# Kernel optimization log

Hardware: AMD Instinct MI355X
Metric: run time of the kernel (lower is better)

## Reference

```python
import jax, jax.numpy as jnp
import numpy as np

N_NODES = 100000
N_EDGES = 1600000
EMBED_DIM = 64


def setup_inputs() -> dict:
    key = jax.random.key(0)
    k1, k2, k3, k4 = jax.random.split(key, 4)
    ego_embeddings = jax.random.normal(k1, (N_NODES, EMBED_DIM), dtype=jnp.float32)
    adj_values = jax.random.uniform(k2, (N_EDGES,), dtype=jnp.float32)
    adj_rows = jax.random.randint(k3, (N_EDGES,), 0, N_NODES, dtype=jnp.int32)
    adj_cols = jax.random.randint(k4, (N_EDGES,), 0, N_NODES, dtype=jnp.int32)
    return {
        "ego_embeddings": ego_embeddings,
        "adj_values": adj_values,
        "adj_rows": adj_rows,
        "adj_cols": adj_cols,
    }


def reference(ego_embeddings, adj_values, adj_rows, adj_cols):
    # out[r, :] = sum_{e : rows[e]==r} values[e] * ego_embeddings[cols[e], :]
    # == tf.sparse.sparse_dense_matmul(adj, ego_embeddings)
    messages = adj_values[:, None] * ego_embeddings[adj_cols]  # [E, D]
    out = jax.ops.segment_sum(messages, adj_rows, num_segments=N_NODES)  # [N, D]
    return out
```

## Files before the change

kernel.cpp:

```cpp
#include <hip/hip_runtime.h>

#define N_NODES 100000
#define N_EDGES 1600000
#define EMBED_DIM 64

#define RPB 256
#define NBKT ((N_NODES + RPB - 1) / RPB)
#define CAP 4608
#define TILE 4096
#define NTILE ((N_EDGES + TILE - 1) / TILE)
#define OVCAP 8192

__global__ __launch_bounds__(512) void k_binA(const int* __restrict__ rows,
                                              const int* __restrict__ cols,
                                              const float* __restrict__ vals,
                                              int* __restrict__ gcur,
                                              int2* __restrict__ packed,
                                              int* __restrict__ ov_cnt,
                                              int4* __restrict__ ov) {
    __shared__ int hist[NBKT];
    __shared__ int off[NBKT];
    __shared__ int cur[NBKT];
    __shared__ int gbase[NBKT];
    __shared__ int wsum[8];
    __shared__ int stotal;
    __shared__ int2 stage[TILE];
    __shared__ int dg[TILE];
    const int tid = threadIdx.x;
    const int lane = tid & 63;
    const int wid = tid >> 6;
    const int e0 = blockIdx.x * TILE;

    for (int i = tid; i < NBKT; i += 512) hist[i] = 0;
    __syncthreads();

    for (int i = tid; i < TILE; i += 512) {
        int e = e0 + i;
        if (e < N_EDGES) atomicAdd(&hist[rows[e] >> 8], 1);
    }
    __syncthreads();

    int v = (tid < NBKT) ? hist[tid] : 0;
    int incl = v;
    for (int o = 1; o < 64; o <<= 1) {
        int t = __shfl_up(incl, o, 64);
        if (lane >= o) incl += t;
    }
    if (lane == 63) wsum[wid] = incl;
    __syncthreads();
    if (wid == 0 && lane < 8) {
        int s = wsum[lane];
        int si = s;
        for (int o = 1; o < 8; o <<= 1) {
            int t = __shfl_up(si, o, 64);
            if (lane >= o) si += t;
        }
        wsum[lane] = si - s;
        if (lane == 7) stotal = si;
    }
    __syncthreads();
    int excl = incl - v + wsum[wid];
    if (tid < NBKT) { off[tid] = excl; cur[tid] = excl; }

    for (int b = tid; b < NBKT; b += 512) {
        int c = hist[b];
        gbase[b] = c ? atomicAdd(&gcur[b], c) : 0;
    }
    __syncthreads();

    for (int i = tid; i < TILE; i += 512) {
        int e = e0 + i;
        if (e < N_EDGES) {
            int r = rows[e];
            int b = r >> 8;
            int p = atomicAdd(&cur[b], 1);
            stage[p] = make_int2(((r & (RPB - 1)) << 17) | cols[e],
                                 __float_as_int(vals[e]));
            int d = gbase[b] + (p - off[b]);
            dg[p] = (d < CAP) ? (b * CAP + d) : (0x40000000 | b);
        }
    }
    __syncthreads();

    int total = stotal;
    for (int j = tid; j < total; j += 512) {
        int d = dg[j];
        int2 ev = stage[j];
        if (d & 0x40000000) {
            int b = d & 0xFFFF;
            int ovi = atomicAdd(ov_cnt, 1);
            if (ovi < OVCAP) {
                int r = b * RPB + (((unsigned)ev.x) >> 17);
                ov[ovi] = make_int4(r, ev.x & 0x1FFFF, ev.y, 0);
            }
        } else {
            packed[d] = ev;
        }
    }
}

__global__ __launch_bounds__(512) void k_binB(const int* __restrict__ gcur,
                                              int2* __restrict__ packed,
                                              int* __restrict__ row_ptr,
                                              int* __restrict__ cnt) {
    __shared__ int2 stage[CAP];
    __shared__ int h[RPB];
    __shared__ int cur[RPB];
    __shared__ int wsum[4];
    const int b = blockIdx.x;
    const int tid = threadIdx.x;
    const int lane = tid & 63;
    const int wid = tid >> 6;
    int n = gcur[b];
    if (n > CAP) n = CAP;
    const int base = b * CAP;

    if (tid < RPB) h[tid] = 0;
    __syncthreads();
    for (int j = tid; j < n; j += 512) {
        int2 e = packed[base + j];
        stage[j] = e;
        atomicAdd(&h[((unsigned)e.x) >> 17], 1);
    }
    __syncthreads();

    int hv = (tid < RPB) ? h[tid] : 0;
    int incl = hv;
    for (int o = 1; o < 64; o <<= 1) {
        int t = __shfl_up(incl, o, 64);
        if (lane >= o) incl += t;
    }
    if (tid < RPB && lane == 63) wsum[wid] = incl;
    __syncthreads();
    if (wid == 0 && lane < 4) {
        int s = wsum[lane];
        int si = s;
        for (int o = 1; o < 4; o <<= 1) {
            int t = __shfl_up(si, o, 64);
            if (lane >= o) si += t;
        }
        wsum[lane] = si - s;
    }
    __syncthreads();
    if (tid < RPB) {
        int ofs = incl - hv + wsum[wid];
        cur[tid] = ofs;
        int r = b * RPB + tid;
        if (r < N_NODES) {
            row_ptr[r] = base + ofs;
            cnt[r] = hv;
        }
    }
    __syncthreads();

    for (int j = tid; j < n; j += 512) {
        int2 e = stage[j];
        int lr = ((unsigned)e.x) >> 17;
        int p = atomicAdd(&cur[lr], 1);
        packed[base + p] = e;
    }
}

__global__ __launch_bounds__(256) void k_gather(const float* __restrict__ x,
                                                const int* __restrict__ row_ptr,
                                                const int* __restrict__ cnt,
                                                const int* __restrict__ pw,
                                                float* __restrict__ out) {
    int wid = (blockIdx.x * 256 + threadIdx.x) >> 6;
    int lane = threadIdx.x & 63;
    if (wid >= N_NODES) return;
    int beg = row_ptr[wid];
    int deg = cnt[wid];
    float acc = 0.f;
    int done = 0;
    while (done < deg) {
        int win = deg - done;
        if (win > 32) win = 32;
        int w = 0;
        if (lane < 2 * win) w = pw[2 * (beg + done) + lane];
        for (int k0 = 0; k0 < win; k0 += 16) {
#pragma unroll
            for (int k = 0; k < 16; ++k) {
                int kk = k0 + k;
                int cpack = __builtin_amdgcn_readlane(w, 2 * kk);
                float v = __int_as_float(__builtin_amdgcn_readlane(w, 2 * kk + 1));
                acc += v * x[(cpack & 0x1FFFF) * EMBED_DIM + lane];
            }
        }
        done += win;
    }
    out[wid * EMBED_DIM + lane] = acc;
}

__global__ __launch_bounds__(256) void k_overflow(const float* __restrict__ x,
                                                  const int* __restrict__ ov_cnt,
                                                  const int4* __restrict__ ov,
                                                  float* __restrict__ out) {
    int n = *ov_cnt;
    if (n > OVCAP) n = OVCAP;
    int lane = threadIdx.x & 63;
    int wglobal = (blockIdx.x * 256 + threadIdx.x) >> 6;
    for (int i = wglobal; i < n; i += 64 * 4) {
        int4 e = ov[i];
        atomicAdd(&out[e.x * EMBED_DIM + lane],
                  __int_as_float(e.z) * x[e.y * EMBED_DIM + lane]);
    }
}

__global__ __launch_bounds__(256) void spmm_scatter_kernel(
    const float* __restrict__ x, const float* __restrict__ vals,
    const int* __restrict__ rows, const int* __restrict__ cols,
    float* __restrict__ out) {
    const int wave_in_block = threadIdx.x >> 6;
    const int lane = threadIdx.x & 63;
    const int e = blockIdx.x * 4 + wave_in_block;
    if (e >= N_EDGES) return;
    const float m = vals[e] * x[cols[e] * EMBED_DIM + lane];
    atomicAdd(&out[rows[e] * EMBED_DIM + lane], m);
}

extern "C" void kernel_launch(void* const* d_in, const int* in_sizes, int n_in,
                              void* d_out, int out_size, void* d_ws, size_t ws_size,
                              hipStream_t stream) {
    const float* x    = (const float*)d_in[0];
    const float* vals = (const float*)d_in[1];
    const int*   rows = (const int*)d_in[2];
    const int*   cols = (const int*)d_in[3];
    float* out = (float*)d_out;

    const size_t packed_b = (size_t)NBKT * CAP * 8;
    const size_t ov_b     = (size_t)OVCAP * 16;
    const size_t need = packed_b + ov_b + ((size_t)NBKT + 1 + 2 * (size_t)N_NODES) * 4;
    if (ws_size < need) {
        hipMemsetAsync(out, 0, (size_t)out_size * sizeof(float), stream);
        spmm_scatter_kernel<<<(N_EDGES + 3) / 4, 256, 0, stream>>>(x, vals, rows, cols, out);
        return;
    }

    int2* packed  = (int2*)d_ws;
    int4* ov      = (int4*)((char*)d_ws + packed_b);
    int*  gcur    = (int*)((char*)d_ws + packed_b + ov_b);
    int*  ov_cnt  = gcur + NBKT;
    int*  row_ptr = ov_cnt + 1;
    int*  cnt     = row_ptr + N_NODES;

    hipMemsetAsync(gcur, 0, ((size_t)NBKT + 1) * sizeof(int), stream);

    k_binA<<<NTILE, 512, 0, stream>>>(rows, cols, vals, gcur, packed, ov_cnt, ov);
    k_binB<<<NBKT, 512, 0, stream>>>(gcur, packed, row_ptr, cnt);
    k_gather<<<(N_NODES * 64 + 255) / 256, 256, 0, stream>>>(x, row_ptr, cnt, (const int*)packed, out);
    k_overflow<<<64, 256, 0, stream>>>(x, ov_cnt, ov, out);
}
```

Before: 173.0 us.

## Replace two-pass bucket sort with per-row fixed-capacity slots via global atomics

Adds a flat path that gives every row a fixed 32-entry slot array. A single scatter kernel places each edge in its row's slot using a per-row global atomic counter, and edges past the capacity go to an overflow list. The gather then reads each row's slots directly. This removes the two-stage shared-memory bucket sort (k_binA/k_binB) and its extra pass over packed data. In exchange it needs a larger workspace, makes scattered global atomics and writes, and drops edges if the overflow list fills.

Result: slower. 256.9 us (+48.5%).

```diff
diff --git a/kernel.cpp b/kernel.cpp
--- a/kernel.cpp
+++ b/kernel.cpp
@@ -3,13 +3,73 @@
 #define N_NODES 100000
 #define N_EDGES 1600000
 #define EMBED_DIM 64
+
+#define CAP_ROW 32
+#define OVCAP 8192
 
 #define RPB 256
 #define NBKT ((N_NODES + RPB - 1) / RPB)
 #define CAP 4608
 #define TILE 4096
 #define NTILE ((N_EDGES + TILE - 1) / TILE)
-#define OVCAP 8192
+
+__global__ __launch_bounds__(256) void k_scatter_flat(const int* __restrict__ rows,
+                                                      const int* __restrict__ cols,
+                                                      const float* __restrict__ vals,
+                                                      int* __restrict__ cnt,
+                                                      int2* __restrict__ packed,
+                                                      int* __restrict__ ov_cnt,
+                                                      int4* __restrict__ ov) {
+    for (int e = blockIdx.x * 256 + threadIdx.x; e < N_EDGES; e += 256 * 2048) {
+        int r = rows[e];
+        int p = atomicAdd(&cnt[r], 1);
+        if (p < CAP_ROW) {
+            packed[(size_t)r * CAP_ROW + p] = make_int2(cols[e], __float_as_int(vals[e]));
+        } else {
+            int ovi = atomicAdd(ov_cnt, 1);
+            if (ovi < OVCAP) ov[ovi] = make_int4(r, cols[e], __float_as_int(vals[e]), 0);
+        }
+    }
+}
+
+__global__ __launch_bounds__(256) void k_gather_flat(const float* __restrict__ x,
+                                                     const int* __restrict__ cnt,
+                                                     const int* __restrict__ pw,
+                                                     float* __restrict__ out) {
+    int wid = (blockIdx.x * 256 + threadIdx.x) >> 6;
+    int lane = threadIdx.x & 63;
+    if (wid >= N_NODES) return;
+    int deg = cnt[wid];
+    if (deg > CAP_ROW) deg = CAP_ROW;
+    int w = 0;
+    if (lane < 2 * deg) w = pw[2 * CAP_ROW * wid + lane];
+    float acc = 0.f;
+    for (int k0 = 0; k0 < deg; k0 += 16) {
+#pragma unroll
+        for (int k = 0; k < 16; ++k) {
+            int kk = k0 + k;
+            int cpack = __builtin_amdgcn_readlane(w, 2 * kk);
+            float v = __int_as_float(__builtin_amdgcn_readlane(w, 2 * kk + 1));
+            acc += v * x[(cpack & 0x1FFFF) * EMBED_DIM + lane];
+        }
+    }
+    out[wid * EMBED_DIM + lane] = acc;
+}
+
+__global__ __launch_bounds__(256) void k_overflow(const float* __restrict__ x,
+                                                  const int* __restrict__ ov_cnt,
+                                                  const int4* __restrict__ ov,
+                                                  float* __restrict__ out) {
+    int n = *ov_cnt;
+    if (n > OVCAP) n = OVCAP;
+    int lane = threadIdx.x & 63;
+    int wglobal = (blockIdx.x * 256 + threadIdx.x) >> 6;
+    for (int i = wglobal; i < n; i += 64 * 4) {
+        int4 e = ov[i];
+        atomicAdd(&out[e.x * EMBED_DIM + lane],
+                  __int_as_float(e.z) * x[e.y * EMBED_DIM + lane]);
+    }
+}
 
 __global__ __launch_bounds__(512) void k_binA(const int* __restrict__ rows,
                                               const int* __restrict__ cols,
@@ -192,21 +252,6 @@
     out[wid * EMBED_DIM + lane] = acc;
 }
 
-__global__ __launch_bounds__(256) void k_overflow(const float* __restrict__ x,
-                                                  const int* __restrict__ ov_cnt,
-                                                  const int4* __restrict__ ov,
-                                                  float* __restrict__ out) {
-    int n = *ov_cnt;
-    if (n > OVCAP) n = OVCAP;
-    int lane = threadIdx.x & 63;
-    int wglobal = (blockIdx.x * 256 + threadIdx.x) >> 6;
-    for (int i = wglobal; i < n; i += 64 * 4) {
-        int4 e = ov[i];
-        atomicAdd(&out[e.x * EMBED_DIM + lane],
-                  __int_as_float(e.z) * x[e.y * EMBED_DIM + lane]);
-    }
-}
-
 __global__ __launch_bounds__(256) void spmm_scatter_kernel(
     const float* __restrict__ x, const float* __restrict__ vals,
     const int* __restrict__ rows, const int* __restrict__ cols,
@@ -228,8 +273,23 @@
     const int*   cols = (const int*)d_in[3];
     float* out = (float*)d_out;
 
+    const size_t flat_packed_b = (size_t)N_NODES * CAP_ROW * 8;
+    const size_t ov_b          = (size_t)OVCAP * 16;
+    const size_t flat_need = flat_packed_b + ov_b + ((size_t)N_NODES + 1) * 4;
+    if (ws_size >= flat_need) {
+        int2* packed = (int2*)d_ws;
+        int4* ov     = (int4*)((char*)d_ws + flat_packed_b);
+        int*  cnt    = (int*)((char*)d_ws + flat_packed_b + ov_b);
+        int*  ov_cnt = cnt + N_NODES;
+
+        hipMemsetAsync(cnt, 0, ((size_t)N_NODES + 1) * sizeof(int), stream);
+        k_scatter_flat<<<2048, 256, 0, stream>>>(rows, cols, vals, cnt, packed, ov_cnt, ov);
+        k_gather_flat<<<(N_NODES * 64 + 255) / 256, 256, 0, stream>>>(x, cnt, (const int*)packed, out);
+        k_overflow<<<64, 256, 0, stream>>>(x, ov_cnt, ov, out);
+        return;
+    }
+
     const size_t packed_b = (size_t)NBKT * CAP * 8;
-    const size_t ov_b     = (size_t)OVCAP * 16;
     const size_t need = packed_b + ov_b + ((size_t)NBKT + 1 + 2 * (size_t)N_NODES) * 4;
     if (ws_size < need) {
         hipMemsetAsync(out, 0, (size_t)out_size * sizeof(float), stream);
```

## Fuse bucket sort and row gather into one kernel using LDS staging

Applied to the files above, without the earlier changes.

Merges the per-bucket counting sort (k_binB) with the gather kernel. Each 1024-thread block loads its bucket into registers, builds a row histogram, scatters the edges into LDS sorted by row, then each wave walks 16 rows and reads edge data straight from LDS. This removes the global write-back of sorted edges, the row_ptr/cnt arrays and one kernel launch. In exchange, only 391 blocks run the gather phase, so there is less parallelism for the random x reads, and the large LDS footprint limits occupancy.

New measurement: 177.4 us. 1.03x slower.

```diff
diff --git a/kernel.cpp b/kernel.cpp
--- a/kernel.cpp
+++ b/kernel.cpp
@@ -10,6 +10,9 @@
 #define TILE 4096
 #define NTILE ((N_EDGES + TILE - 1) / TILE)
 #define OVCAP 8192
+
+#define BG_THREADS 1024
+#define EPT ((CAP + BG_THREADS - 1) / BG_THREADS)
 
 __global__ __launch_bounds__(512) void k_binA(const int* __restrict__ rows,
                                               const int* __restrict__ cols,
@@ -99,12 +102,13 @@
     }
 }
 
-__global__ __launch_bounds__(512) void k_binB(const int* __restrict__ gcur,
-                                              int2* __restrict__ packed,
-                                              int* __restrict__ row_ptr,
-                                              int* __restrict__ cnt) {
+__global__ __launch_bounds__(BG_THREADS) void k_bg(const float* __restrict__ x,
+                                                   const int* __restrict__ gcur,
+                                                   const int2* __restrict__ packed,
+                                                   float* __restrict__ out) {
     __shared__ int2 stage[CAP];
     __shared__ int h[RPB];
+    __shared__ int ofs[RPB];
     __shared__ int cur[RPB];
     __shared__ int wsum[4];
     const int b = blockIdx.x;
@@ -117,10 +121,20 @@
 
     if (tid < RPB) h[tid] = 0;
     __syncthreads();
-    for (int j = tid; j < n; j += 512) {
-        int2 e = packed[base + j];
-        stage[j] = e;
-        atomicAdd(&h[((unsigned)e.x) >> 17], 1);
+
+    int2 ereg[EPT];
+    int lr[EPT];
+#pragma unroll
+    for (int jj = 0; jj < EPT; ++jj) {
+        int j = tid + jj * BG_THREADS;
+        lr[jj] = -1;
+        if (j < n) {
+            int2 e = packed[base + j];
+            ereg[jj] = e;
+            int r = ((unsigned)e.x) >> 17;
+            lr[jj] = r;
+            atomicAdd(&h[r], 1);
+        }
     }
     __syncthreads();
 
@@ -143,53 +157,48 @@
     }
     __syncthreads();
     if (tid < RPB) {
-        int ofs = incl - hv + wsum[wid];
-        cur[tid] = ofs;
-        int r = b * RPB + tid;
-        if (r < N_NODES) {
-            row_ptr[r] = base + ofs;
-            cnt[r] = hv;
-        }
-    }
-    __syncthreads();
-
-    for (int j = tid; j < n; j += 512) {
-        int2 e = stage[j];
-        int lr = ((unsigned)e.x) >> 17;
-        int p = atomicAdd(&cur[lr], 1);
-        packed[base + p] = e;
-    }
-}
-
-__global__ __launch_bounds__(256) void k_gather(const float* __restrict__ x,
-                                                const int* __restrict__ row_ptr,
-                                                const int* __restrict__ cnt,
-                                                const int* __restrict__ pw,
-                                                float* __restrict__ out) {
-    int wid = (blockIdx.x * 256 + threadIdx.x) >> 6;
-    int lane = threadIdx.x & 63;
-    if (wid >= N_NODES) return;
-    int beg = row_ptr[wid];
-    int deg = cnt[wid];
-    float acc = 0.f;
-    int done = 0;
-    while (done < deg) {
-        int win = deg - done;
-        if (win > 32) win = 32;
-        int w = 0;
-        if (lane < 2 * win) w = pw[2 * (beg + done) + lane];
-        for (int k0 = 0; k0 < win; k0 += 16) {
+        int o2 = incl - hv + wsum[wid];
+        ofs[tid] = o2;
+        cur[tid] = o2;
+    }
+    __syncthreads();
+
 #pragma unroll
-            for (int k = 0; k < 16; ++k) {
-                int kk = k0 + k;
-                int cpack = __builtin_amdgcn_readlane(w, 2 * kk);
-                float v = __int_as_float(__builtin_amdgcn_readlane(w, 2 * kk + 1));
-                acc += v * x[(cpack & 0x1FFFF) * EMBED_DIM + lane];
+    for (int jj = 0; jj < EPT; ++jj) {
+        if (lr[jj] >= 0) {
+            int p = atomicAdd(&cur[lr[jj]], 1);
+            stage[p] = ereg[jj];
+        }
+    }
+    __syncthreads();
+
+    const int* sw = (const int*)stage;
+    for (int i = 0; i < 16; ++i) {
+        int r = wid * 16 + i;
+        int grow = b * RPB + r;
+        if (grow >= N_NODES) break;
+        int deg = h[r];
+        int beg = ofs[r];
+        float acc = 0.f;
+        int done = 0;
+        while (done < deg) {
+            int win = deg - done;
+            if (win > 32) win = 32;
+            int w = 0;
+            if (lane < 2 * win) w = sw[((beg + done) << 1) + lane];
+            for (int k0 = 0; k0 < win; k0 += 16) {
+#pragma unroll
+                for (int k = 0; k < 16; ++k) {
+                    int kk = k0 + k;
+                    int cpack = __builtin_amdgcn_readlane(w, 2 * kk);
+                    float v = __int_as_float(__builtin_amdgcn_readlane(w, 2 * kk + 1));
+                    acc += v * x[(cpack & 0x1FFFF) * EMBED_DIM + lane];
+                }
             }
-        }
-        done += win;
-    }
-    out[wid * EMBED_DIM + lane] = acc;
+            done += win;
+        }
+        out[(size_t)grow * EMBED_DIM + lane] = acc;
+    }
 }
 
 __global__ __launch_bounds__(256) void k_overflow(const float* __restrict__ x,
@@ -230,7 +239,7 @@
 
     const size_t packed_b = (size_t)NBKT * CAP * 8;
     const size_t ov_b     = (size_t)OVCAP * 16;
-    const size_t need = packed_b + ov_b + ((size_t)NBKT + 1 + 2 * (size_t)N_NODES) * 4;
+    const size_t need = packed_b + ov_b + ((size_t)NBKT + 1) * 4;
     if (ws_size < need) {
         hipMemsetAsync(out, 0, (size_t)out_size * sizeof(float), stream);
         spmm_scatter_kernel<<<(N_EDGES + 3) / 4, 256, 0, stream>>>(x, vals, rows, cols, out);
@@ -241,13 +250,10 @@
     int4* ov      = (int4*)((char*)d_ws + packed_b);
     int*  gcur    = (int*)((char*)d_ws + packed_b + ov_b);
     int*  ov_cnt  = gcur + NBKT;
-    int*  row_ptr = ov_cnt + 1;
-    int*  cnt     = row_ptr + N_NODES;
 
     hipMemsetAsync(gcur, 0, ((size_t)NBKT + 1) * sizeof(int), stream);
 
     k_binA<<<NTILE, 512, 0, stream>>>(rows, cols, vals, gcur, packed, ov_cnt, ov);
-    k_binB<<<NBKT, 512, 0, stream>>>(gcur, packed, row_ptr, cnt);
-    k_gather<<<(N_NODES * 64 + 255) / 256, 256, 0, stream>>>(x, row_ptr, cnt, (const int*)packed, out);
+    k_bg<<<NBKT, BG_THREADS, 0, stream>>>(x, gcur, (const int2*)packed, out);
     k_overflow<<<64, 256, 0, stream>>>(x, ov_cnt, ov, out);
 }
```
